# Kernel optimization log

Measured on AMD Instinct MI355X. Metric: run time of the kernel, lower is better.

The kernel has to match this reference:

```python
import math
import jax, jax.numpy as jnp
import numpy as np

G, NP, L = 256, 24, 3            # graphs, atoms per graph, GPS layers
C, TDIM, NFREQ, NT = 256, 256, 10, 100
EDIM = NFREQ * 2 * 3 + 9         # SinusoidsEmbedding.dim + lattice_input_dim = 69
N = G * NP                       # 6144 nodes
H = 4                            # attention heads


def _silu(x):
    return x * jax.nn.sigmoid(x)


def _bn(x, g, b):
    # BatchNorm1d, training-mode batch statistics (biased var), eps=1e-5
    m = x.mean(0)
    v = ((x - m) ** 2).mean(0)
    return (x - m) * jax.lax.rsqrt(v + 1e-5) * g + b


def _forward(t, frac_coords, lattice, type_emb, node_align_W, node_align_b,
             gine_edge_W, gine_edge_b, gine_W1, gine_b1, gine_W2, gine_b2,
             attn_in_W, attn_in_b, attn_out_W, attn_out_b,
             mlp_W1, mlp_b1, mlp_W2, mlp_b2,
             bn1_g, bn1_b, bn2_g, bn2_b, bn3_g, bn3_b, ln_g, ln_b,
             tro_W1, tro_b1, tro_W2, tro_b2,
             lat_W1, lat_b1, lat_W2, lat_b2, lat_W3,
             fc_W1, fc_b1, fc_W2, fc_b2, fc_W3,
             atom_types, node2graph, edge_src, edge_dst):
    # sinusoidal time embedding [G, TDIM], repeated per node
    half = TDIM // 2
    tf = jnp.exp(jnp.arange(half, dtype=jnp.float32) * (-math.log(10000.0) / (half - 1)))
    te = t[:, None] * tf[None, :]
    te = jnp.concatenate([jnp.sin(te), jnp.cos(te)], -1)
    time_emb = jnp.repeat(te, NP, axis=0)                      # [N, TDIM]
    x = jnp.concatenate([type_emb[atom_types], time_emb], 1) @ node_align_W + node_align_b

    # edge features: sinusoids of periodic frac diff + per-graph lattice
    fd = (frac_coords[edge_dst] - frac_coords[edge_src]) % 1.0  # [E,3]
    sf = 2.0 * math.pi * jnp.arange(NFREQ, dtype=jnp.float32)
    emb = (fd[..., None] * sf).reshape(-1, 3 * NFREQ)
    eattr = jnp.concatenate([jnp.sin(emb), jnp.cos(emb), lattice[node2graph[edge_src]]], 1)

    scale = 1.0 / math.sqrt(C // H)
    for l in range(L):
        # --- GINEConv: gather -> relu(x_j + edge_emb) -> scatter-add -> MLP ---
        eemb = eattr @ gine_edge_W[l] + gine_edge_b[l]          # [E, C]
        msg = jax.nn.relu(x[edge_src] + eemb)
        aggr = jax.ops.segment_sum(msg, edge_dst, num_segments=N)
        z = x + aggr                                            # (1+eps)*x, eps=0
        z = _silu(z @ gine_W1[l] + gine_b1[l]) @ gine_W2[l] + gine_b2[l]
        h1 = _bn(z + x, bn1_g[l], bn1_b[l])
        # --- dense-batched multihead self-attention (all graphs have NP nodes) ---
        xd = x.reshape(G, NP, C)
        qkv = xd @ attn_in_W[l] + attn_in_b[l]
        q, k, v = jnp.split(qkv, 3, axis=-1)
        q = q.reshape(G, NP, H, C // H).transpose(0, 2, 1, 3)
        k = k.reshape(G, NP, H, C // H).transpose(0, 2, 1, 3)
        v = v.reshape(G, NP, H, C // H).transpose(0, 2, 1, 3)
        a = jax.nn.softmax(jnp.einsum('ghqd,ghkd->ghqk', q, k) * scale, axis=-1)
        o = jnp.einsum('ghqk,ghkd->ghqd', a, v).transpose(0, 2, 1, 3).reshape(G, NP, C)
        o = (o @ attn_out_W[l] + attn_out_b[l]).reshape(N, C)
        h2 = _bn(o + x, bn2_g[l], bn2_b[l])
        # --- combine + MLP (GPSConv default: ReLU, dropout=0) ---
        out = h1 + h2
        out = out + jax.nn.relu(out @ mlp_W1[l] + mlp_b1[l]) @ mlp_W2[l] + mlp_b2[l]
        x = _bn(out, bn3_g[l], bn3_b[l])

    # final LayerNorm over feature dim
    m = x.mean(-1, keepdims=True)
    v = ((x - m) ** 2).mean(-1, keepdims=True)
    hn = (x - m) * jax.lax.rsqrt(v + 1e-5) * ln_g + ln_b

    # scatter-mean graph pooling
    cnt = jax.ops.segment_sum(jnp.ones((N, 1), hn.dtype), node2graph, num_segments=G)
    gf = jax.ops.segment_sum(hn, node2graph, num_segments=G) / cnt

    types_pred = _silu(hn @ tro_W1 + tro_b1) @ tro_W2 + tro_b2
    lattice_pred = _silu(_silu(gf @ lat_W1 + lat_b1) @ lat_W2 + lat_b2) @ lat_W3
    frac_pred = _silu(_silu(hn @ fc_W1 + fc_b1) @ fc_W2 + fc_b2) @ fc_W3
    return types_pred, lattice_pred, frac_pred


def setup_inputs() -> dict:
    key = jax.random.key(0)
    ki = iter(jax.random.split(key, 40))

    def nrm(shape, s=0.02):
        return jax.random.normal(next(ki), shape, jnp.float32) * s

    # block-diagonal fully-connected edges, dense_to_sparse row-major order
    g = np.repeat(np.arange(G), NP * NP)
    i = np.tile(np.repeat(np.arange(NP), NP), G)
    j = np.tile(np.tile(np.arange(NP), NP), G)
    inp = {
        "t": jax.random.uniform(next(ki), (G,), jnp.float32),
        "frac_coords": jax.random.uniform(next(ki), (N, 3), jnp.float32),
        "lattice": nrm((G, 9), 1.0),
        "type_emb": nrm((NT, C)),
        "node_align_W": nrm((C + TDIM, C)), "node_align_b": jnp.zeros((C,), jnp.float32),
        "gine_edge_W": nrm((L, EDIM, C)), "gine_edge_b": jnp.zeros((L, C), jnp.float32),
        "gine_W1": nrm((L, C, C)), "gine_b1": jnp.zeros((L, C), jnp.float32),
        "gine_W2": nrm((L, C, C)), "gine_b2": jnp.zeros((L, C), jnp.float32),
        "attn_in_W": nrm((L, C, 3 * C)), "attn_in_b": jnp.zeros((L, 3 * C), jnp.float32),
        "attn_out_W": nrm((L, C, C)), "attn_out_b": jnp.zeros((L, C), jnp.float32),
        "mlp_W1": nrm((L, C, 2 * C)), "mlp_b1": jnp.zeros((L, 2 * C), jnp.float32),
        "mlp_W2": nrm((L, 2 * C, C)), "mlp_b2": jnp.zeros((L, C), jnp.float32),
        "bn1_g": jnp.ones((L, C), jnp.float32), "bn1_b": jnp.zeros((L, C), jnp.float32),
        "bn2_g": jnp.ones((L, C), jnp.float32), "bn2_b": jnp.zeros((L, C), jnp.float32),
        "bn3_g": jnp.ones((L, C), jnp.float32), "bn3_b": jnp.zeros((L, C), jnp.float32),
        "ln_g": jnp.ones((C,), jnp.float32), "ln_b": jnp.zeros((C,), jnp.float32),
        "tro_W1": nrm((C, C // 2)), "tro_b1": jnp.zeros((C // 2,), jnp.float32),
        "tro_W2": nrm((C // 2, NT)), "tro_b2": jnp.zeros((NT,), jnp.float32),
        "lat_W1": nrm((C, C // 2)), "lat_b1": jnp.zeros((C // 2,), jnp.float32),
        "lat_W2": nrm((C // 2, C // 4)), "lat_b2": jnp.zeros((C // 4,), jnp.float32),
        "lat_W3": nrm((C // 4, 9)),
        "fc_W1": nrm((C, C // 2)), "fc_b1": jnp.zeros((C // 2,), jnp.float32),
        "fc_W2": nrm((C // 2, C // 4)), "fc_b2": jnp.zeros((C // 4,), jnp.float32),
        "fc_W3": nrm((C // 4, 3)),
        "atom_types": jax.random.randint(next(ki), (N,), 0, NT, jnp.int32),
        "node2graph": jnp.asarray(np.repeat(np.arange(G), NP), jnp.int32),
        "edge_src": jnp.asarray(g * NP + i, jnp.int32),
        "edge_dst": jnp.asarray(g * NP + j, jnp.int32),
    }
    return inp


def reference(t, frac_coords, lattice, type_emb, node_align_W, node_align_b,
              gine_edge_W, gine_edge_b, gine_W1, gine_b1, gine_W2, gine_b2,
              attn_in_W, attn_in_b, attn_out_W, attn_out_b,
              mlp_W1, mlp_b1, mlp_W2, mlp_b2,
              bn1_g, bn1_b, bn2_g, bn2_b, bn3_g, bn3_b, ln_g, ln_b,
              tro_W1, tro_b1, tro_W2, tro_b2,
              lat_W1, lat_b1, lat_W2, lat_b2, lat_W3,
              fc_W1, fc_b1, fc_W2, fc_b2, fc_W3,
              atom_types, node2graph, edge_src, edge_dst):
    return _forward(t, frac_coords, lattice, type_emb, node_align_W, node_align_b,
                    gine_edge_W, gine_edge_b, gine_W1, gine_b1, gine_W2, gine_b2,
                    attn_in_W, attn_in_b, attn_out_W, attn_out_b,
                    mlp_W1, mlp_b1, mlp_W2, mlp_b2,
                    bn1_g, bn1_b, bn2_g, bn2_b, bn3_g, bn3_b, ln_g, ln_b,
                    tro_W1, tro_b1, tro_W2, tro_b2,
                    lat_W1, lat_b1, lat_W2, lat_b2, lat_W3,
                    fc_W1, fc_b1, fc_W2, fc_b2, fc_W3,
                    atom_types, node2graph, edge_src, edge_dst)
```

## Files before the change

### kernel.cpp

```cpp
#include <hip/hip_runtime.h>
#include <hip/hip_bf16.h>
#include <math.h>

#define GG 256
#define NP 24
#define LL 3
#define CC 256
#define NN (GG*NP)
#define HH 4
#define DH 64

typedef __hip_bfloat16 bf;
typedef __attribute__((ext_vector_type(8))) short bfrag;
typedef __attribute__((ext_vector_type(4))) float ffrag;

__device__ __forceinline__ short pk(float x) {
    union { bf h; short s; } u; u.h = __float2bfloat16(x); return u.s;
}
__device__ __forceinline__ float b2f_s(short x) {
    union { short s; bf h; } u; u.s = x; return __bfloat162float(u.h);
}

__global__ void detect_int_k(const unsigned int* __restrict__ at, int* flags) {
    __shared__ int ok;
    if (threadIdx.x == 0) ok = 1;
    __syncthreads();
    if (at[2 * threadIdx.x + 1] != 0u) ok = 0;
    __syncthreads();
    if (threadIdx.x == 0) flags[0] = ok;
}

__global__ void signal_k(float* out, int n, float val) {
    int i = blockIdx.x * 256 + threadIdx.x;
    if (i < n) out[i] = val;
}

struct TArgs {
    const float* src[9];
    long dstOff[9];
    int K[9], N[9], L[9];
    int blk0[10];
};
__global__ void transp_all(TArgs a, bf* __restrict__ wt) {
    int bid = blockIdx.x;
    int s = 0;
    while (s < 8 && bid >= a.blk0[s + 1]) ++s;
    long idx = (long)(bid - a.blk0[s]) * 256 + threadIdx.x;
    int KN = a.K[s] * a.N[s];
    long sz = (long)KN * a.L[s];
    if (idx >= sz) return;
    int l = (int)(idx / KN);
    int rem = (int)(idx % KN);
    int k = rem / a.N[s], n = rem % a.N[s];
    wt[a.dstOff[s] + (long)l * KN + (long)n * a.K[s] + k] =
        __float2bfloat16(a.src[s][idx]);
}

__global__ void prep_gew(const float* __restrict__ geW, short* __restrict__ wh,
                         short* __restrict__ wl) {
    int idx = blockIdx.x * 256 + threadIdx.x;
    if (idx >= 49152) return;
    int k = idx & 63;
    int n = (idx >> 6) & 127;
    int half = (idx >> 13) & 1;
    int l = idx >> 14;
    float v = (k < 60) ? geW[(long)l * 69 * 256 + (long)k * 256 + half * 128 + n] : 0.f;
    short hi = pk(v);
    short lo = pk(v - b2f_s(hi));
    wh[idx] = hi;
    wl[idx] = lo;
}

#define ETAB_ELEMS (GG * 24 * 24 * 64)
__global__ void prep_etab(const float* __restrict__ frac, short* __restrict__ eh,
                          short* __restrict__ el) {
    int idx = blockIdx.x * 256 + threadIdx.x;
    if (idx >= ETAB_ELEMS) return;
    int k = idx & 63;
    int rem = idx >> 6;
    int i = rem % 24;
    int rem2 = rem / 24;
    int j = rem2 % 24;
    int g = rem2 / 24;
    float val = 0.f;
    if (k < 60) {
        int r = (k < 30) ? k : k - 30;
        int d = r / 10, f = r % 10;
        float fd = frac[g * 72 + j * 3 + d] - frac[g * 72 + i * 3 + d];
        fd -= floorf(fd);
        float ang = 6.283185307179586f * (float)f * fd;
        val = (k < 30) ? sinf(ang) : cosf(ang);
    }
    short hi = pk(val);
    eh[idx] = hi;
    el[idx] = pk(val - b2f_s(hi));
}

__global__ void build_A(const float* __restrict__ t, const float* __restrict__ type_emb,
                        const unsigned int* __restrict__ atoms,
                        float* __restrict__ A, const int* __restrict__ flags) {
    int i64 = flags[0];
    int idx = blockIdx.x * 256 + threadIdx.x;
    if (idx >= NN * 512) return;
    int n = idx >> 9;
    int k = idx & 511;
    if (k < 256) {
        int a = i64 ? (int)atoms[2 * n] : (int)atoms[n];
        A[idx] = type_emb[(long)a * CC + k];
    } else {
        int d = k - 256;
        int g = n / NP;
        float tv = t[g];
        int dd = (d < 128) ? d : d - 128;
        float tf = expf(dd * (-9.210340371976184f / 127.0f));
        float ang = tv * tf;
        A[idx] = (d < 128) ? sinf(ang) : cosf(ang);
    }
}

__global__ __launch_bounds__(256) void gemm_mfma(
        const float* __restrict__ A, const bf* __restrict__ Wt,
        const float* __restrict__ bias, const float* __restrict__ res,
        float* __restrict__ C, int M, int K, int N, int act) {
    __shared__ __align__(16) short As[32 * 40];
    __shared__ __align__(16) short Bs[64 * 40];
    int tid = threadIdx.x;
    int lane = tid & 63, w = tid >> 6;
    int wm = w & 1, wn = w >> 1;
    int m0 = blockIdx.x * 32, n0 = blockIdx.y * 64;
    ffrag acc[2] = {};
    int sa_m = tid >> 3, sa_k = (tid & 7) << 2;
    int sb_n = tid >> 2, sb_k = (tid & 3) << 3;
    int fr_row = lane & 15, fr_k = (lane >> 4) << 3;

    for (int k0 = 0; k0 < K; k0 += 32) {
        const float* Ap = A + (long)(m0 + sa_m) * K + k0 + sa_k;
        float4 a1 = *(const float4*)Ap;
        float4 b1 = *(const float4*)(Wt + (long)(n0 + sb_n) * K + k0 + sb_k);
        __syncthreads();
        short av0 = pk(a1.x), av1 = pk(a1.y), av2 = pk(a1.z), av3 = pk(a1.w);
        short* ap = &As[sa_m * 40 + sa_k];
        ap[0] = av0; ap[1] = av1; ap[2] = av2; ap[3] = av3;
        *(float4*)(&Bs[sb_n * 40 + sb_k]) = b1;
        __syncthreads();
        bfrag af = *(const bfrag*)(&As[(wm * 16 + fr_row) * 40 + fr_k]);
        bfrag bg0 = *(const bfrag*)(&Bs[(wn * 32 + fr_row) * 40 + fr_k]);
        bfrag bg1 = *(const bfrag*)(&Bs[(wn * 32 + 16 + fr_row) * 40 + fr_k]);
        acc[0] = __builtin_amdgcn_mfma_f32_16x16x32_bf16(af, bg0, acc[0], 0, 0, 0);
        acc[1] = __builtin_amdgcn_mfma_f32_16x16x32_bf16(af, bg1, acc[1], 0, 0, 0);
    }

    int mbase = (lane >> 4) << 2;
#pragma unroll
    for (int nt = 0; nt < 2; ++nt) {
        int n = n0 + wn * 32 + nt * 16 + (lane & 15);
        float bv = bias ? bias[n] : 0.f;
#pragma unroll
        for (int r = 0; r < 4; ++r) {
            int m = m0 + wm * 16 + mbase + r;
            float v = acc[nt][r] + bv;
            if (act == 1) v = fmaxf(v, 0.f);
            else if (act == 2) v = v / (1.f + expf(-v));
            if (res) v += res[(long)m * N + n];
            C[(long)m * N + n] = v;
        }
    }
}

__global__ __launch_bounds__(256) void gemm_k(
        const float* __restrict__ A, const float* __restrict__ W,
        const float* __restrict__ bias, const float* __restrict__ res,
        float* __restrict__ Cf, int M, int K, int Nc, int act) {
    __shared__ __align__(16) float Asf[32][64];
    __shared__ __align__(16) float Bsf[32][64];
    int tid = threadIdx.x;
    int tx = tid & 15, ty = tid >> 4;
    int m0 = blockIdx.x * 64, n0 = blockIdx.y * 64;
    float acc[4][4] = {{0.f}};
    int am = tid >> 2;
    int ak = (tid & 3) << 3;
    int bk = tid >> 4;
    int bn = (tid & 15) << 2;

    for (int k0 = 0; k0 < K; k0 += 32) {
        const float* Ap = A + (long)(m0 + am) * K + k0 + ak;
        float4 a1 = *(const float4*)Ap;
        float4 a2 = *(const float4*)(Ap + 4);
        float w1[4], w2[4];
#pragma unroll
        for (int u = 0; u < 4; ++u) {
            int n = n0 + bn + u;
            w1[u] = (n < Nc) ? W[(long)(k0 + bk) * Nc + n] : 0.f;
            w2[u] = (n < Nc) ? W[(long)(k0 + bk + 16) * Nc + n] : 0.f;
        }
        __syncthreads();
        Asf[ak + 0][am] = a1.x; Asf[ak + 1][am] = a1.y;
        Asf[ak + 2][am] = a1.z; Asf[ak + 3][am] = a1.w;
        Asf[ak + 4][am] = a2.x; Asf[ak + 5][am] = a2.y;
        Asf[ak + 6][am] = a2.z; Asf[ak + 7][am] = a2.w;
#pragma unroll
        for (int u = 0; u < 4; ++u) {
            Bsf[bk][bn + u] = w1[u];
            Bsf[bk + 16][bn + u] = w2[u];
        }
        __syncthreads();
#pragma unroll
        for (int k = 0; k < 32; ++k) {
            float4 a = *(const float4*)(&Asf[k][ty << 2]);
            float4 b = *(const float4*)(&Bsf[k][tx << 2]);
            acc[0][0] += a.x * b.x; acc[0][1] += a.x * b.y; acc[0][2] += a.x * b.z; acc[0][3] += a.x * b.w;
            acc[1][0] += a.y * b.x; acc[1][1] += a.y * b.y; acc[1][2] += a.y * b.z; acc[1][3] += a.y * b.w;
            acc[2][0] += a.z * b.x; acc[2][1] += a.z * b.y; acc[2][2] += a.z * b.z; acc[2][3] += a.z * b.w;
            acc[3][0] += a.w * b.x; acc[3][1] += a.w * b.y; acc[3][2] += a.w * b.z; acc[3][3] += a.w * b.w;
        }
    }
#pragma unroll
    for (int i = 0; i < 4; ++i) {
        int m = m0 + (ty << 2) + i;
#pragma unroll
        for (int j = 0; j < 4; ++j) {
            int n = n0 + (tx << 2) + j;
            if (n >= Nc) continue;
            float v = acc[i][j];
            if (bias) v += bias[n];
            if (act == 1) v = fmaxf(v, 0.f);
            else if (act == 2) v = v / (1.f + expf(-v));
            if (res) v += res[(long)m * Nc + n];
            Cf[(long)m * Nc + n] = v;
        }
    }
}

#define MF(a, b, c) c = __builtin_amdgcn_mfma_f32_16x16x32_bf16(a, b, c, 0, 0, 0)

typedef __attribute__((address_space(1))) const void gv_t;
typedef __attribute__((address_space(3))) void lv_t;

__device__ __forceinline__ void stage_etile(const short* __restrict__ ej_h,
                                            const short* __restrict__ ej_l,
                                            short* lds_base, int w, int lane) {
    {
        int c = w;
        const short* src = (c < 3) ? (ej_h + c * 512) : (ej_l + (c - 3) * 512);
        int doff = (c < 3) ? c * 512 : 2048 + (c - 3) * 512;
        __builtin_amdgcn_global_load_lds((gv_t*)(src + lane * 8),
                                         (lv_t*)(lds_base + doff), 16, 0, 0);
    }
    if (w < 2) {
        int c = w + 4;
        const short* src = ej_l + (c - 3) * 512;
        int doff = 2048 + (c - 3) * 512;
        __builtin_amdgcn_global_load_lds((gv_t*)(src + lane * 8),
                                         (lv_t*)(lds_base + doff), 16, 0, 0);
    }
}

__global__ __launch_bounds__(256, 4) void gine4(
        const float* __restrict__ x,
        const float* __restrict__ lattice, const float* __restrict__ geW,
        const float* __restrict__ geb, const short* __restrict__ gewt_h,
        const short* __restrict__ gewt_l, const short* __restrict__ et_h,
        const short* __restrict__ et_l, float* __restrict__ z, int l) {
    __shared__ __align__(16) float xls[24 * 132];
    __shared__ float basel[128];
    __shared__ __align__(16) short ebuf[8192];

    int tid = threadIdx.x;
    int lane = tid & 63, w = tid >> 6, quad = lane >> 4, l16 = lane & 15;
    int g = blockIdx.x >> 2;
    int half = (blockIdx.x >> 1) & 1;
    int jh = blockIdx.x & 1;

    {
        const float4* xg = (const float4*)x;
        for (int idx = tid; idx < 768; idx += 256) {
            int i = idx >> 5, c4 = idx & 31;
            ((float4*)(xls + i * 132))[c4] =
                xg[((long)(g * NP + i) * CC + half * 128) / 4 + c4];
        }
    }
    if (tid < 128) {
        int cg = half * 128 + tid;
        float bv = geb[(long)l * CC + cg];
#pragma unroll
        for (int q = 0; q < 9; ++q)
            bv += lattice[(long)g * 9 + q] * geW[(long)l * 69 * 256 + (long)(60 + q) * 256 + cg];
        basel[tid] = bv;
    }

    bfrag bh00, bh01, bh10, bh11, bl00, bl01, bl10, bl11;
    {
        long base = (long)(l * 2 + half) * 8192;
        int nrow0 = w * 32 + l16;
        int nrow1 = w * 32 + 16 + l16;
        const short* p0h = gewt_h + base + nrow0 * 64 + quad * 8;
        const short* p1h = gewt_h + base + nrow1 * 64 + quad * 8;
        const short* p0l = gewt_l + base + nrow0 * 64 + quad * 8;
        const short* p1l = gewt_l + base + nrow1 * 64 + quad * 8;
        bh00 = *(const bfrag*)(p0h);      bh01 = *(const bfrag*)(p0h + 32);
        bh10 = *(const bfrag*)(p1h);      bh11 = *(const bfrag*)(p1h + 32);
        bl00 = *(const bfrag*)(p0l);      bl01 = *(const bfrag*)(p0l + 32);
        bl10 = *(const bfrag*)(p1l);      bl11 = *(const bfrag*)(p1l + 32);
    }

    const short* ehg = et_h + (long)g * (24 * 24 * 64);
    const short* elg = et_l + (long)g * (24 * 24 * 64);
    int j0 = jh * 12;

    stage_etile(ehg + (long)j0 * 1536, elg + (long)j0 * 1536, ebuf, w, lane);
    __syncthreads();

    float bse0 = basel[w * 32 + l16];
    float bse1 = basel[w * 32 + 16 + l16];

    int cur = 0;
    for (int jc = 0; jc < 12; ++jc) {
        int j = j0 + jc;
        if (jc < 11) {
            stage_etile(ehg + (long)(j + 1) * 1536, elg + (long)(j + 1) * 1536,
                        ebuf + (cur ^ 1) * 4096, w, lane);
        }

        const short* eb = ebuf + cur * 4096;
        int r0 = l16 * 64 + quad * 8;
        int r1 = (16 + l16) * 64 + quad * 8;
        bfrag ah00 = *(const bfrag*)(eb + r0);
        bfrag ah01 = *(const bfrag*)(eb + r0 + 32);
        bfrag ah10 = *(const bfrag*)(eb + r1);
        bfrag ah11 = *(const bfrag*)(eb + r1 + 32);
        bfrag al00 = *(const bfrag*)(eb + 2048 + r0);
        bfrag al01 = *(const bfrag*)(eb + 2048 + r0 + 32);
        bfrag al10 = *(const bfrag*)(eb + 2048 + r1);
        bfrag al11 = *(const bfrag*)(eb + 2048 + r1 + 32);

        ffrag a00 = {}, a01 = {}, a10 = {}, a11 = {};
        MF(ah00, bh00, a00); MF(ah00, bl00, a00); MF(al00, bh00, a00);
        MF(ah00, bh10, a01); MF(ah00, bl10, a01); MF(al00, bh10, a01);
        MF(ah01, bh01, a00); MF(ah01, bl01, a00); MF(al01, bh01, a00);
        MF(ah01, bh11, a01); MF(ah01, bl11, a01); MF(al01, bh11, a01);
        MF(ah10, bh00, a10); MF(ah10, bl00, a10); MF(al10, bh00, a10);
        MF(ah10, bh10, a11); MF(ah10, bl10, a11); MF(al10, bh10, a11);
        MF(ah11, bh01, a10); MF(ah11, bl01, a10); MF(al11, bh01, a10);
        MF(ah11, bh11, a11); MF(ah11, bl11, a11); MF(al11, bh11, a11);

#pragma unroll
        for (int nt = 0; nt < 2; ++nt) {
            int cl = w * 32 + nt * 16 + l16;
            float bse = nt ? bse1 : bse0;
            ffrag am0 = nt ? a01 : a00;
            ffrag am1 = nt ? a11 : a10;
            float part = 0.f;
            {
                int ibase = quad * 4;
#pragma unroll
                for (int r = 0; r < 4; ++r) {
                    float xv = xls[(ibase + r) * 132 + cl];
                    part += fmaxf(xv + bse + am0[r], 0.f);
                }
            }
            if (quad < 2) {
                int ibase = 16 + quad * 4;
#pragma unroll
                for (int r = 0; r < 4; ++r) {
                    float xv = xls[(ibase + r) * 132 + cl];
                    part += fmaxf(xv + bse + am1[r], 0.f);
                }
            }
            part += __shfl_xor(part, 16);
            part += __shfl_xor(part, 32);
            if (lane < 16)
                z[(long)(g * NP + j) * CC + half * 128 + cl] = xls[j * 132 + cl] + part;
        }
        __syncthreads();
        cur ^= 1;
    }
}

__global__ void bn_stats1(const float* __restrict__ in, float* __restrict__ part) {
    int c = threadIdx.x, b = blockIdx.x;
    float s = 0.f, q = 0.f;
    for (int r = 0; r < 64; ++r) {
        float v = in[(long)(b * 64 + r) * CC + c];
        s += v; q += v * v;
    }
    part[b * 512 + c] = s;
    part[b * 512 + 256 + c] = q;
}
__global__ __launch_bounds__(256) void bn_apply2(
        const float* __restrict__ in, const float* __restrict__ part,
        const float* __restrict__ gma, const float* __restrict__ bta,
        const float* __restrict__ add, float* __restrict__ out) {
    int c = threadIdx.x;
    float s = 0.f, q = 0.f;
    for (int b = 0; b < 96; ++b) { s += part[b * 512 + c]; q += part[b * 512 + 256 + c]; }
    float m = s / (float)NN;
    float var = q / (float)NN - m * m;
    float stats_c = m;
    float stats_rs = rsqrtf(var + 1e-5f);
    float gc = gma[c], bc = bta[c];
    for (int r = blockIdx.x; r < NN; r += 768) {
        long idx = (long)r * CC + c;
        float v = (in[idx] - stats_c) * stats_rs * gc + bc;
        if (add) v += add[idx];
        out[idx] = v;
    }
}

__global__ __launch_bounds__(256, 2) void attn2(const float* __restrict__ qkv,
                                                float* __restrict__ o) {
    __shared__ __align__(16) float Kl[24 * 4 * 68];
    __shared__ __align__(16) float Vl[24 * 4 * 68];
    __shared__ float S[4 * 24 * 25];
    int tid = threadIdx.x, g = blockIdx.x;

    const float4* qkv4 = (const float4*)(qkv + (long)g * NP * 768);
    for (int idx = tid; idx < 24 * 128; idx += 256) {
        int row = idx >> 7;
        int c4 = idx & 127;
        int isV = c4 >> 6;
        int cc = c4 & 63;
        int h = cc >> 4, d4 = cc & 15;
        float4 val = qkv4[row * 192 + 64 + c4];
        float* dst = (isV ? Vl : Kl) + (row * 4 + h) * 68 + d4 * 4;
        *(float4*)dst = val;
    }
    __syncthreads();

    if (tid < 96) {
        int h = tid & 3, i = tid >> 2;
        const float4* qp = (const float4*)(qkv + ((long)(g * NP + i)) * 768 + h * 64);
        float4 q[16];
#pragma unroll
        for (int k = 0; k < 16; ++k) q[k] = qp[k];
        float sc[24];
        float mx = -1e30f;
        for (int j = 0; j < 24; ++j) {
            const float4* kp = (const float4*)(Kl + (j * 4 + h) * 68);
            float da = 0.f, db = 0.f;
#pragma unroll
            for (int k = 0; k < 16; k += 2) {
                float4 kv = kp[k];
                da += q[k].x * kv.x; da += q[k].y * kv.y;
                da += q[k].z * kv.z; da += q[k].w * kv.w;
                float4 kv2 = kp[k + 1];
                db += q[k + 1].x * kv2.x; db += q[k + 1].y * kv2.y;
                db += q[k + 1].z * kv2.z; db += q[k + 1].w * kv2.w;
            }
            float s = (da + db) * 0.125f;
            sc[j] = s;
            mx = fmaxf(mx, s);
        }
        float sum = 0.f;
#pragma unroll
        for (int j = 0; j < 24; ++j) { float p = expf(sc[j] - mx); sc[j] = p; sum += p; }
        float inv = 1.f / sum;
#pragma unroll
        for (int j = 0; j < 24; ++j) S[(h * 24 + i) * 25 + j] = sc[j] * inv;
    }
    __syncthreads();

    int h = tid >> 6, d = tid & 63;
    for (int i = 0; i < 24; ++i) {
        const float* Sp = S + (h * 24 + i) * 25;
        float a0 = 0.f, a1 = 0.f;
#pragma unroll
        for (int j = 0; j < 24; j += 2) {
            a0 += Sp[j] * Vl[(j * 4 + h) * 68 + d];
            a1 += Sp[j + 1] * Vl[((j + 1) * 4 + h) * 68 + d];
        }
        o[(long)(g * NP + i) * CC + h * 64 + d] = a0 + a1;
    }
}

__global__ __launch_bounds__(256) void ln_kernel(const float* __restrict__ x,
        const float* __restrict__ gma, const float* __restrict__ bta,
        float* __restrict__ out) {
    __shared__ float red[256];
    int n = blockIdx.x, c = threadIdx.x;
    float v = x[(long)n * CC + c];
    red[c] = v;
    __syncthreads();
    for (int s = 128; s > 0; s >>= 1) { if (c < s) red[c] += red[c + s]; __syncthreads(); }
    float m = red[0] * (1.f / 256.f);
    __syncthreads();
    float dv = v - m;
    red[c] = dv * dv;
    __syncthreads();
    for (int s = 128; s > 0; s >>= 1) { if (c < s) red[c] += red[c + s]; __syncthreads(); }
    float var = red[0] * (1.f / 256.f);
    out[(long)n * CC + c] = dv * rsqrtf(var + 1e-5f) * gma[c] + bta[c];
}

__global__ void pool_kernel(const float* __restrict__ hn, float* __restrict__ gf) {
    int g = blockIdx.x, c = threadIdx.x;
    float s = 0.f;
    for (int j = 0; j < NP; ++j) s += hn[(long)(g * NP + j) * CC + c];
    gf[g * CC + c] = s * (1.f / 24.f);
}

__global__ __launch_bounds__(256) void lat_head(
        const float* __restrict__ gf, const float* __restrict__ W1,
        const float* __restrict__ b1, const float* __restrict__ W2,
        const float* __restrict__ b2, const float* __restrict__ W3,
        float* __restrict__ out) {
    __shared__ float gfl[256];
    __shared__ float h1[128];
    __shared__ float h2[64];
    int g = blockIdx.x, t = threadIdx.x;
    gfl[t] = gf[(long)g * 256 + t];
    __syncthreads();
    if (t < 128) {
        float acc = 0.f;
        for (int k = 0; k < 256; ++k) acc += gfl[k] * W1[k * 128 + t];
        float v = acc;
        v += b1[t];
        v = v / (1.f + expf(-v));
        h1[t] = v;
    }
    __syncthreads();
    if (t < 64) {
        float acc = 0.f;
        for (int k = 0; k < 128; ++k) acc += h1[k] * W2[k * 64 + t];
        float v = acc;
        v += b2[t];
        v = v / (1.f + expf(-v));
        h2[t] = v;
    }
    __syncthreads();
    if (t < 9) {
        float acc = 0.f;
        for (int k = 0; k < 64; ++k) acc += h2[k] * W3[k * 9 + t];
        out[(long)g * 9 + t] = acc;
    }
}

static void gemm(hipStream_t st, const float* A, const float* W, const float* bias,
                 const float* res, float* Cf, int M, int K, int Nc, int act) {
    dim3 grid(M / 64, (Nc + 63) / 64);
    gemm_k<<<grid, 256, 0, st>>>(A, W, bias, res, Cf, M, K, Nc, act);
}

static void gemmM(hipStream_t st, const float* A, const bf* Wt, const float* bias,
                  const float* res, float* Cf, int M, int K, int N, int act) {
    dim3 grid(M / 32, N / 64);
    gemm_mfma<<<grid, 256, 0, st>>>(A, Wt, bias, res, Cf, M, K, N, act);
}

static void run_bn(hipStream_t st, const float* in, float* part, float* stats,
                   const float* g_, const float* b_, const float* add, float* out) {
    (void)stats;
    bn_stats1<<<96, 256, 0, st>>>(in, part);
    bn_apply2<<<768, 256, 0, st>>>(in, part, g_, b_, add, out);
}

extern "C" void kernel_launch(void* const* d_in, const int* in_sizes, int n_in,
                              void* d_out, int out_size, void* d_ws, size_t ws_size,
                              hipStream_t stream) {
    float* out = (float*)d_out;
    int sigN = out_size < 256 ? out_size : 256;

    static const int EXP_SIZES[46] = {
        256, 18432, 2304, 25600, 131072, 256, 52992, 768, 196608, 768,
        196608, 768, 589824, 2304, 196608, 768, 393216, 1536, 393216, 768,
        768, 768, 768, 768, 768, 768, 256, 256, 32768, 128,
        12800, 100, 32768, 128, 8192, 64, 576, 32768, 128, 8192,
        64, 192, 6144, 6144, 147456, 147456 };
    if (n_in != 46) { signal_k<<<1, 256, 0, stream>>>(out, sigN, 3000.f + 8.f * n_in); return; }
    for (int i = 0; i < 46; ++i)
        if (in_sizes[i] != EXP_SIZES[i]) { signal_k<<<1, 256, 0, stream>>>(out, sigN, 512.f + 8.f * i); return; }
    if (out_size != NN * 100 + GG * 9 + NN * 3) { signal_k<<<1, 256, 0, stream>>>(out, sigN, 7777.f); return; }

    char* base = (char*)d_ws;
    int* flags = (int*)base;
    float* f32a = (float*)(base + 256);
    float* x  = f32a;
    float* s1 = x  + (size_t)NN * 256;
    float* s2 = s1 + (size_t)NN * 256;
    float* big = s2 + (size_t)NN * 256;
    float* s3 = big + (size_t)NN * 512;
    float* part = big + (size_t)NN * 768;
    float* stats = part + 96 * 512;
    float* gf  = stats + 512;
    float* l1b = gf + GG * 256;
    float* l2b = l1b + GG * 128;
    bf* wt = (bf*)(l2b + GG * 64);
    const long O_NA = 0, O_G1 = 131072, O_G2 = 327680, O_AI = 524288,
               O_AO = 1114112, O_M1 = 1310720, O_M2 = 1703936,
               O_TRO = 2097152, O_FC = 2129920, WT_TOT = 2162688;
    short* gewt_h = (short*)(wt + WT_TOT);
    short* gewt_l = gewt_h + 49152;
    short* et_h = gewt_l + 49152;
    short* et_l = et_h + (ETAB_ELEMS + 1024);
    size_t REQ = 256 + ((size_t)NN * 1536 + 96 * 512 + 512 + GG * 448) * 4
               + WT_TOT * 2 + 49152 * 2 * 2
               + ((size_t)ETAB_ELEMS + 1024) * 2 * 2;
    if (ws_size < REQ) { signal_k<<<1, 256, 0, stream>>>(out, sigN, 9999.f); return; }

    const float* t       = (const float*)d_in[0];
    const float* frac    = (const float*)d_in[1];
    const float* lattice = (const float*)d_in[2];
    const float* type_emb = (const float*)d_in[3];

    detect_int_k<<<1, 256, 0, stream>>>((const unsigned int*)d_in[42], flags);

    {
        TArgs ta;
        const int srcIdx[9] = {4, 8, 10, 12, 14, 16, 18, 28, 37};
        const long dof[9]  = {O_NA, O_G1, O_G2, O_AI, O_AO, O_M1, O_M2, O_TRO, O_FC};
        const int Ks[9] = {512, 256, 256, 256, 256, 256, 512, 256, 256};
        const int Ns[9] = {256, 256, 256, 768, 256, 512, 256, 128, 128};
        const int Ls[9] = {1, 3, 3, 3, 3, 3, 3, 1, 1};
        int blk = 0;
        for (int s = 0; s < 9; ++s) {
            ta.src[s] = (const float*)d_in[srcIdx[s]];
            ta.dstOff[s] = dof[s];
            ta.K[s] = Ks[s]; ta.N[s] = Ns[s]; ta.L[s] = Ls[s];
            ta.blk0[s] = blk;
            blk += (Ks[s] * Ns[s] * Ls[s] + 255) / 256;
        }
        ta.blk0[9] = blk;
        transp_all<<<blk, 256, 0, stream>>>(ta, wt);
    }
    prep_gew<<<192, 256, 0, stream>>>((const float*)d_in[6], gewt_h, gewt_l);
    prep_etab<<<(ETAB_ELEMS + 255) / 256, 256, 0, stream>>>(frac, et_h, et_l);

    build_A<<<(NN * 512 + 255) / 256, 256, 0, stream>>>(t, type_emb,
        (const unsigned int*)d_in[42], big, flags);
    gemmM(stream, big, wt + O_NA, (const float*)d_in[5], nullptr, x, NN, 512, 256, 0);

    for (int l = 0; l < LL; ++l) {
        gine4<<<GG * 4, 256, 0, stream>>>(x, lattice,
            (const float*)d_in[6], (const float*)d_in[7], gewt_h, gewt_l,
            et_h, et_l, s1, l);
        gemmM(stream, s1, wt + O_G1 + (long)l * 65536, (const float*)d_in[9]  + l * 256, nullptr, s2, NN, 256, 256, 2);
        gemmM(stream, s2, wt + O_G2 + (long)l * 65536, (const float*)d_in[11] + l * 256, x, s3, NN, 256, 256, 0);
        run_bn(stream, s3, part, stats, (const float*)d_in[20] + l * 256, (const float*)d_in[21] + l * 256, nullptr, s2);
        gemmM(stream, x, wt + O_AI + (long)l * 196608, (const float*)d_in[13] + l * 768, nullptr, big, NN, 256, 768, 0);
        attn2<<<GG, 256, 0, stream>>>(big, s1);
        gemmM(stream, s1, wt + O_AO + (long)l * 65536, (const float*)d_in[15] + l * 256, x, s3, NN, 256, 256, 0);
        run_bn(stream, s3, part, stats, (const float*)d_in[22] + l * 256, (const float*)d_in[23] + l * 256, s2, s1);
        gemmM(stream, s1, wt + O_M1 + (long)l * 131072, (const float*)d_in[17] + l * 512, nullptr, big, NN, 256, 512, 1);
        gemmM(stream, big, wt + O_M2 + (long)l * 131072, (const float*)d_in[19] + l * 256, s1, s3, NN, 512, 256, 0);
        run_bn(stream, s3, part, stats, (const float*)d_in[24] + l * 256, (const float*)d_in[25] + l * 256, nullptr, x);
    }

    ln_kernel<<<NN, 256, 0, stream>>>(x, (const float*)d_in[26], (const float*)d_in[27], s1);
    pool_kernel<<<GG, 256, 0, stream>>>(s1, gf);

    gemmM(stream, s1, wt + O_TRO, (const float*)d_in[29], nullptr, s2, NN, 256, 128, 2);
    gemm(stream, s2, (const float*)d_in[30], (const float*)d_in[31], nullptr, out, NN, 128, 100, 0);
    lat_head<<<GG, 256, 0, stream>>>(gf, (const float*)d_in[32], (const float*)d_in[33],
        (const float*)d_in[34], (const float*)d_in[35], (const float*)d_in[36],
        out + (size_t)NN * 100);
    gemmM(stream, s1, wt + O_FC, (const float*)d_in[38], nullptr, s2, NN, 256, 128, 2);
    gemm(stream, s2, (const float*)d_in[39], (const float*)d_in[40], nullptr, s3, NN, 128, 64, 2);
    gemm(stream, s3, (const float*)d_in[41], nullptr, nullptr, out + (size_t)NN * 100 + GG * 9, NN, 64, 3, 0);
}
```

Measured before the change: 749.5 us.

## Double-buffer MFMA GEMM with direct LDS weight loads and fuse head kernels

The MFMA GEMM now processes K in steps of 64 with double-buffered LDS tiles, loading weights via global_load_lds while the next A tile is prefetched into registers. This overlaps memory with compute and halves the barriers. Separately, the two prep kernels are merged, mean pooling is folded into lat_head, and the TRO and FC first-layer GEMMs are fused into one N=256 GEMM with a split bias. The fused GEMM relies on the two transposed weight blocks being contiguous, and LDS use increases.

```diff
diff --git a/kernel.cpp b/kernel.cpp
--- a/kernel.cpp
+++ b/kernel.cpp
@@ -20,6 +20,9 @@
 __device__ __forceinline__ float b2f_s(short x) {
     union { short s; bf h; } u; u.s = x; return __bfloat162float(u.h);
 }
+
+typedef __attribute__((address_space(1))) const void gv_t;
+typedef __attribute__((address_space(3))) void lv_t;
 
 __global__ void detect_int_k(const unsigned int* __restrict__ at, int* flags) {
     __shared__ int ok;
@@ -56,44 +59,45 @@
         __float2bfloat16(a.src[s][idx]);
 }
 
-__global__ void prep_gew(const float* __restrict__ geW, short* __restrict__ wh,
-                         short* __restrict__ wl) {
-    int idx = blockIdx.x * 256 + threadIdx.x;
-    if (idx >= 49152) return;
-    int k = idx & 63;
-    int n = (idx >> 6) & 127;
-    int half = (idx >> 13) & 1;
-    int l = idx >> 14;
-    float v = (k < 60) ? geW[(long)l * 69 * 256 + (long)k * 256 + half * 128 + n] : 0.f;
-    short hi = pk(v);
-    short lo = pk(v - b2f_s(hi));
-    wh[idx] = hi;
-    wl[idx] = lo;
-}
-
 #define ETAB_ELEMS (GG * 24 * 24 * 64)
-__global__ void prep_etab(const float* __restrict__ frac, short* __restrict__ eh,
-                          short* __restrict__ el) {
-    int idx = blockIdx.x * 256 + threadIdx.x;
-    if (idx >= ETAB_ELEMS) return;
-    int k = idx & 63;
-    int rem = idx >> 6;
-    int i = rem % 24;
-    int rem2 = rem / 24;
-    int j = rem2 % 24;
-    int g = rem2 / 24;
-    float val = 0.f;
-    if (k < 60) {
-        int r = (k < 30) ? k : k - 30;
-        int d = r / 10, f = r % 10;
-        float fd = frac[g * 72 + j * 3 + d] - frac[g * 72 + i * 3 + d];
-        fd -= floorf(fd);
-        float ang = 6.283185307179586f * (float)f * fd;
-        val = (k < 30) ? sinf(ang) : cosf(ang);
-    }
-    short hi = pk(val);
-    eh[idx] = hi;
-    el[idx] = pk(val - b2f_s(hi));
+__global__ void prep_gewtab(const float* __restrict__ geW, short* __restrict__ wh,
+                            short* __restrict__ wl, const float* __restrict__ frac,
+                            short* __restrict__ eh, short* __restrict__ el) {
+    int bid = blockIdx.x;
+    if (bid < 192) {
+        int idx = bid * 256 + threadIdx.x;
+        if (idx >= 49152) return;
+        int k = idx & 63;
+        int n = (idx >> 6) & 127;
+        int half = (idx >> 13) & 1;
+        int l = idx >> 14;
+        float v = (k < 60) ? geW[(long)l * 69 * 256 + (long)k * 256 + half * 128 + n] : 0.f;
+        short hi = pk(v);
+        short lo = pk(v - b2f_s(hi));
+        wh[idx] = hi;
+        wl[idx] = lo;
+    } else {
+        int idx = (bid - 192) * 256 + threadIdx.x;
+        if (idx >= ETAB_ELEMS) return;
+        int k = idx & 63;
+        int rem = idx >> 6;
+        int i = rem % 24;
+        int rem2 = rem / 24;
+        int j = rem2 % 24;
+        int g = rem2 / 24;
+        float val = 0.f;
+        if (k < 60) {
+            int r = (k < 30) ? k : k - 30;
+            int d = r / 10, f = r % 10;
+            float fd = frac[g * 72 + j * 3 + d] - frac[g * 72 + i * 3 + d];
+            fd -= floorf(fd);
+            float ang = 6.283185307179586f * (float)f * fd;
+            val = (k < 30) ? sinf(ang) : cosf(ang);
+        }
+        short hi = pk(val);
+        eh[idx] = hi;
+        el[idx] = pk(val - b2f_s(hi));
+    }
 }
 
 __global__ void build_A(const float* __restrict__ t, const float* __restrict__ type_emb,
@@ -120,41 +124,73 @@
 
 __global__ __launch_bounds__(256) void gemm_mfma(
         const float* __restrict__ A, const bf* __restrict__ Wt,
-        const float* __restrict__ bias, const float* __restrict__ res,
+        const float* __restrict__ bias, const float* __restrict__ bias2,
+        const float* __restrict__ res,
         float* __restrict__ C, int M, int K, int N, int act) {
-    __shared__ __align__(16) short As[32 * 40];
-    __shared__ __align__(16) short Bs[64 * 40];
+    __shared__ __align__(16) short As[2][32 * 72];
+    __shared__ __align__(16) short Bs[2][2][64 * 32];
     int tid = threadIdx.x;
     int lane = tid & 63, w = tid >> 6;
     int wm = w & 1, wn = w >> 1;
     int m0 = blockIdx.x * 32, n0 = blockIdx.y * 64;
     ffrag acc[2] = {};
-    int sa_m = tid >> 3, sa_k = (tid & 7) << 2;
-    int sb_n = tid >> 2, sb_k = (tid & 3) << 3;
-    int fr_row = lane & 15, fr_k = (lane >> 4) << 3;
-
-    for (int k0 = 0; k0 < K; k0 += 32) {
-        const float* Ap = A + (long)(m0 + sa_m) * K + k0 + sa_k;
+    int sa_m = tid >> 3, sa_k = (tid & 7) << 3;
+    int fr_row = lane & 15, quad = lane >> 4, fr_k = quad << 3;
+    int brow = w * 16 + (lane >> 2);
+    int bko = (lane & 3) << 3;
+    const short* wsrc = (const short*)Wt + (long)(n0 + brow) * K + bko;
+
+    {
+        const float* Ap = A + (long)(m0 + sa_m) * K + sa_k;
         float4 a1 = *(const float4*)Ap;
-        float4 b1 = *(const float4*)(Wt + (long)(n0 + sb_n) * K + k0 + sb_k);
+        float4 a2 = *(const float4*)(Ap + 4);
+        __builtin_amdgcn_global_load_lds((gv_t*)(wsrc), (lv_t*)(&Bs[0][0][w * 512]), 16, 0, 0);
+        __builtin_amdgcn_global_load_lds((gv_t*)(wsrc + 32), (lv_t*)(&Bs[0][1][w * 512]), 16, 0, 0);
+        short* ap = &As[0][sa_m * 72 + sa_k];
+        ap[0] = pk(a1.x); ap[1] = pk(a1.y); ap[2] = pk(a1.z); ap[3] = pk(a1.w);
+        ap[4] = pk(a2.x); ap[5] = pk(a2.y); ap[6] = pk(a2.z); ap[7] = pk(a2.w);
+    }
+    __syncthreads();
+
+    int nk = K >> 6;
+    int cur = 0;
+    for (int i = 0; i < nk; ++i) {
+        float4 a1n, a2n;
+        bool more = (i + 1) < nk;
+        if (more) {
+            int kn = (i + 1) << 6;
+            __builtin_amdgcn_global_load_lds((gv_t*)(wsrc + kn),
+                (lv_t*)(&Bs[cur ^ 1][0][w * 512]), 16, 0, 0);
+            __builtin_amdgcn_global_load_lds((gv_t*)(wsrc + kn + 32),
+                (lv_t*)(&Bs[cur ^ 1][1][w * 512]), 16, 0, 0);
+            const float* Ap = A + (long)(m0 + sa_m) * K + kn + sa_k;
+            a1n = *(const float4*)Ap;
+            a2n = *(const float4*)(Ap + 4);
+        }
+        bfrag af0  = *(const bfrag*)(&As[cur][(wm * 16 + fr_row) * 72 + fr_k]);
+        bfrag af1  = *(const bfrag*)(&As[cur][(wm * 16 + fr_row) * 72 + 32 + fr_k]);
+        bfrag bg00 = *(const bfrag*)(&Bs[cur][0][(wn * 32 + fr_row) * 32 + fr_k]);
+        bfrag bg01 = *(const bfrag*)(&Bs[cur][0][(wn * 32 + 16 + fr_row) * 32 + fr_k]);
+        bfrag bg10 = *(const bfrag*)(&Bs[cur][1][(wn * 32 + fr_row) * 32 + fr_k]);
+        bfrag bg11 = *(const bfrag*)(&Bs[cur][1][(wn * 32 + 16 + fr_row) * 32 + fr_k]);
+        acc[0] = __builtin_amdgcn_mfma_f32_16x16x32_bf16(af0, bg00, acc[0], 0, 0, 0);
+        acc[1] = __builtin_amdgcn_mfma_f32_16x16x32_bf16(af0, bg01, acc[1], 0, 0, 0);
+        acc[0] = __builtin_amdgcn_mfma_f32_16x16x32_bf16(af1, bg10, acc[0], 0, 0, 0);
+        acc[1] = __builtin_amdgcn_mfma_f32_16x16x32_bf16(af1, bg11, acc[1], 0, 0, 0);
+        if (more) {
+            short* ap = &As[cur ^ 1][sa_m * 72 + sa_k];
+            ap[0] = pk(a1n.x); ap[1] = pk(a1n.y); ap[2] = pk(a1n.z); ap[3] = pk(a1n.w);
+            ap[4] = pk(a2n.x); ap[5] = pk(a2n.y); ap[6] = pk(a2n.z); ap[7] = pk(a2n.w);
+        }
         __syncthreads();
-        short av0 = pk(a1.x), av1 = pk(a1.y), av2 = pk(a1.z), av3 = pk(a1.w);
-        short* ap = &As[sa_m * 40 + sa_k];
-        ap[0] = av0; ap[1] = av1; ap[2] = av2; ap[3] = av3;
-        *(float4*)(&Bs[sb_n * 40 + sb_k]) = b1;
-        __syncthreads();
-        bfrag af = *(const bfrag*)(&As[(wm * 16 + fr_row) * 40 + fr_k]);
-        bfrag bg0 = *(const bfrag*)(&Bs[(wn * 32 + fr_row) * 40 + fr_k]);
-        bfrag bg1 = *(const bfrag*)(&Bs[(wn * 32 + 16 + fr_row) * 40 + fr_k]);
-        acc[0] = __builtin_amdgcn_mfma_f32_16x16x32_bf16(af, bg0, acc[0], 0, 0, 0);
-        acc[1] = __builtin_amdgcn_mfma_f32_16x16x32_bf16(af, bg1, acc[1], 0, 0, 0);
+        cur ^= 1;
     }
 
     int mbase = (lane >> 4) << 2;
 #pragma unroll
     for (int nt = 0; nt < 2; ++nt) {
         int n = n0 + wn * 32 + nt * 16 + (lane & 15);
-        float bv = bias ? bias[n] : 0.f;
+        float bv = bias ? ((bias2 && n >= 128) ? bias2[n - 128] : bias[n]) : 0.f;
 #pragma unroll
         for (int r = 0; r < 4; ++r) {
             int m = m0 + wm * 16 + mbase + r;
@@ -168,7 +204,7 @@
 }
 
 __global__ __launch_bounds__(256) void gemm_k(
-        const float* __restrict__ A, const float* __restrict__ W,
+        const float* __restrict__ A, int lda, const float* __restrict__ W,
         const float* __restrict__ bias, const float* __restrict__ res,
         float* __restrict__ Cf, int M, int K, int Nc, int act) {
     __shared__ __align__(16) float Asf[32][64];
@@ -183,7 +219,7 @@
     int bn = (tid & 15) << 2;
 
     for (int k0 = 0; k0 < K; k0 += 32) {
-        const float* Ap = A + (long)(m0 + am) * K + k0 + ak;
+        const float* Ap = A + (long)(m0 + am) * lda + k0 + ak;
         float4 a1 = *(const float4*)Ap;
         float4 a2 = *(const float4*)(Ap + 4);
         float w1[4], w2[4];
@@ -232,9 +268,6 @@
 }
 
 #define MF(a, b, c) c = __builtin_amdgcn_mfma_f32_16x16x32_bf16(a, b, c, 0, 0, 0)
-
-typedef __attribute__((address_space(1))) const void gv_t;
-typedef __attribute__((address_space(3))) void lv_t;
 
 __device__ __forceinline__ void stage_etile(const short* __restrict__ ej_h,
                                             const short* __restrict__ ej_l,
@@ -491,15 +524,8 @@
     out[(long)n * CC + c] = dv * rsqrtf(var + 1e-5f) * gma[c] + bta[c];
 }
 
-__global__ void pool_kernel(const float* __restrict__ hn, float* __restrict__ gf) {
-    int g = blockIdx.x, c = threadIdx.x;
-    float s = 0.f;
-    for (int j = 0; j < NP; ++j) s += hn[(long)(g * NP + j) * CC + c];
-    gf[g * CC + c] = s * (1.f / 24.f);
-}
-
 __global__ __launch_bounds__(256) void lat_head(
-        const float* __restrict__ gf, const float* __restrict__ W1,
+        const float* __restrict__ hn, const float* __restrict__ W1,
         const float* __restrict__ b1, const float* __restrict__ W2,
         const float* __restrict__ b2, const float* __restrict__ W3,
         float* __restrict__ out) {
@@ -507,7 +533,11 @@
     __shared__ float h1[128];
     __shared__ float h2[64];
     int g = blockIdx.x, t = threadIdx.x;
-    gfl[t] = gf[(long)g * 256 + t];
+    {
+        float s = 0.f;
+        for (int j = 0; j < NP; ++j) s += hn[(long)(g * NP + j) * CC + t];
+        gfl[t] = s * (1.f / 24.f);
+    }
     __syncthreads();
     if (t < 128) {
         float acc = 0.f;
@@ -534,21 +564,22 @@
     }
 }
 
-static void gemm(hipStream_t st, const float* A, const float* W, const float* bias,
-                 const float* res, float* Cf, int M, int K, int Nc, int act) {
+static void gemm(hipStream_t st, const float* A, int lda, const float* W,
+                 const float* bias, const float* res, float* Cf,
+                 int M, int K, int Nc, int act) {
     dim3 grid(M / 64, (Nc + 63) / 64);
-    gemm_k<<<grid, 256, 0, st>>>(A, W, bias, res, Cf, M, K, Nc, act);
+    gemm_k<<<grid, 256, 0, st>>>(A, lda, W, bias, res, Cf, M, K, Nc, act);
 }
 
 static void gemmM(hipStream_t st, const float* A, const bf* Wt, const float* bias,
-                  const float* res, float* Cf, int M, int K, int N, int act) {
+                  const float* bias2, const float* res, float* Cf,
+                  int M, int K, int N, int act) {
     dim3 grid(M / 32, N / 64);
-    gemm_mfma<<<grid, 256, 0, st>>>(A, Wt, bias, res, Cf, M, K, N, act);
-}
-
-static void run_bn(hipStream_t st, const float* in, float* part, float* stats,
+    gemm_mfma<<<grid, 256, 0, st>>>(A, Wt, bias, bias2, res, Cf, M, K, N, act);
+}
+
+static void run_bn(hipStream_t st, const float* in, float* part,
                    const float* g_, const float* b_, const float* add, float* out) {
-    (void)stats;
     bn_stats1<<<96, 256, 0, st>>>(in, part);
     bn_apply2<<<768, 256, 0, st>>>(in, part, g_, b_, add, out);
 }
@@ -621,38 +652,37 @@
         ta.blk0[9] = blk;
         transp_all<<<blk, 256, 0, stream>>>(ta, wt);
     }
-    prep_gew<<<192, 256, 0, stream>>>((const float*)d_in[6], gewt_h, gewt_l);
-    prep_etab<<<(ETAB_ELEMS + 255) / 256, 256, 0, stream>>>(frac, et_h, et_l);
+    prep_gewtab<<<192 + (ETAB_ELEMS + 255) / 256, 256, 0, stream>>>(
+        (const float*)d_in[6], gewt_h, gewt_l, frac, et_h, et_l);
 
     build_A<<<(NN * 512 + 255) / 256, 256, 0, stream>>>(t, type_emb,
         (const unsigned int*)d_in[42], big, flags);
-    gemmM(stream, big, wt + O_NA, (const float*)d_in[5], nullptr, x, NN, 512, 256, 0);
+    gemmM(stream, big, wt + O_NA, (const float*)d_in[5], nullptr, nullptr, x, NN, 512, 256, 0);
 
     for (int l = 0; l < LL; ++l) {
         gine4<<<GG * 4, 256, 0, stream>>>(x, lattice,
             (const float*)d_in[6], (const float*)d_in[7], gewt_h, gewt_l,
             et_h, et_l, s1, l);
-        gemmM(stream, s1, wt + O_G1 + (long)l * 65536, (const float*)d_in[9]  + l * 256, nullptr, s2, NN, 256, 256, 2);
-        gemmM(stream, s2, wt + O_G2 + (long)l * 65536, (const float*)d_in[11] + l * 256, x, s3, NN, 256, 256, 0);
-        run_bn(stream, s3, part, stats, (const float*)d_in[20] + l * 256, (const float*)d_in[21] + l * 256, nullptr, s2);
-        gemmM(stream, x, wt + O_AI + (long)l * 196608, (const float*)d_in[13] + l * 768, nullptr, big, NN, 256, 768, 0);
+        gemmM(stream, s1, wt + O_G1 + (long)l * 65536, (const float*)d_in[9]  + l * 256, nullptr, nullptr, s2, NN, 256, 256, 2);
+        gemmM(stream, s2, wt + O_G2 + (long)l * 65536, (const float*)d_in[11] + l * 256, nullptr, x, s3, NN, 256, 256, 0);
+        run_bn(stream, s3, part, (const float*)d_in[20] + l * 256, (const float*)d_in[21] + l * 256, nullptr, s2);
+        gemmM(stream, x, wt + O_AI + (long)l * 196608, (const float*)d_in[13] + l * 768, nullptr, nullptr, big, NN, 256, 768, 0);
         attn2<<<GG, 256, 0, stream>>>(big, s1);
-        gemmM(stream, s1, wt + O_AO + (long)l * 65536, (const float*)d_in[15] + l * 256, x, s3, NN, 256, 256, 0);
-        run_bn(stream, s3, part, stats, (const float*)d_in[22] + l * 256, (const float*)d_in[23] + l * 256, s2, s1);
-        gemmM(stream, s1, wt + O_M1 + (long)l * 131072, (const float*)d_in[17] + l * 512, nullptr, big, NN, 256, 512, 1);
-        gemmM(stream, big, wt + O_M2 + (long)l * 131072, (const float*)d_in[19] + l * 256, s1, s3, NN, 512, 256, 0);
-        run_bn(stream, s3, part, stats, (const float*)d_in[24] + l * 256, (const float*)d_in[25] + l * 256, nullptr, x);
+        gemmM(stream, s1, wt + O_AO + (long)l * 65536, (const float*)d_in[15] + l * 256, nullptr, x, s3, NN, 256, 256, 0);
+        run_bn(stream, s3, part, (const float*)d_in[22] + l * 256, (const float*)d_in[23] + l * 256, s2, s1);
+        gemmM(stream, s1, wt + O_M1 + (long)l * 131072, (const float*)d_in[17] + l * 512, nullptr, nullptr, big, NN, 256, 512, 1);
+        gemmM(stream, big, wt + O_M2 + (long)l * 131072, (const float*)d_in[19] + l * 256, nullptr, s1, s3, NN, 512, 256, 0);
+        run_bn(stream, s3, part, (const float*)d_in[24] + l * 256, (const float*)d_in[25] + l * 256, nullptr, x);
     }
 
     ln_kernel<<<NN, 256, 0, stream>>>(x, (const float*)d_in[26], (const float*)d_in[27], s1);
-    pool_kernel<<<GG, 256, 0, stream>>>(s1, gf);
-
-    gemmM(stream, s1, wt + O_TRO, (const float*)d_in[29], nullptr, s2, NN, 256, 128, 2);
-    gemm(stream, s2, (const float*)d_in[30], (const float*)d_in[31], nullptr, out, NN, 128, 100, 0);
-    lat_head<<<GG, 256, 0, stream>>>(gf, (const float*)d_in[32], (const float*)d_in[33],
+
+    gemmM(stream, s1, wt + O_TRO, (const float*)d_in[29], (const float*)d_in[38],
+          nullptr, s2, NN, 256, 256, 2);
+    gemm(stream, s2, 256, (const float*)d_in[30], (const float*)d_in[31], nullptr, out, NN, 128, 100, 0);
+    lat_head<<<GG, 256, 0, stream>>>(s1, (const float*)d_in[32], (const float*)d_in[33],
         (const float*)d_in[34], (const float*)d_in[35], (const float*)d_in[36],
         out + (size_t)NN * 100);
-    gemmM(stream, s1, wt + O_FC, (const float*)d_in[38], nullptr, s2, NN, 256, 128, 2);
-    gemm(stream, s2, (const float*)d_in[39], (const float*)d_in[40], nullptr, s3, NN, 128, 64, 2);
-    gemm(stream, s3, (const float*)d_in[41], nullptr, nullptr, out + (size_t)NN * 100 + GG * 9, NN, 64, 3, 0);
-}
+    gemm(stream, s2 + 128, 256, (const float*)d_in[39], (const float*)d_in[40], nullptr, s3, NN, 128, 64, 2);
+    gemm(stream, s3, 64, (const float*)d_in[41], nullptr, nullptr, out + (size_t)NN * 100 + GG * 9, NN, 64, 3, 0);
+}
```

After: 712.5 us. -4.9%, faster.
